# Performance work log

Hardware: AMD Instinct MI355X
Metric: run time of the kernel (lower is better)

## Reference

```python
import jax, jax.numpy as jnp
import numpy as np

FULL_SCALE = 128.0
R = 0.5
TOPK = 4


def setup_inputs() -> dict:
    key = jax.random.key(0)
    k0, k1, k2, k3, k4 = jax.random.split(key, 5)
    B, Na, Nb, D = 16, 2048, 2048, 512
    coords_a = jax.random.randint(k0, (B, Na, 3), 0, 128, dtype=jnp.int32)
    coords_b = jax.random.randint(k1, (B, Nb, 3), 0, 128, dtype=jnp.int32)
    feats_a = jax.random.normal(k2, (B, Na, D), jnp.float32)
    feats_b = jax.random.normal(k3, (B, Nb, D), jnp.float32)
    W = jax.random.normal(k4, (2 * D, D), jnp.float32) / np.sqrt(2 * D).astype(np.float32)
    bias = jnp.zeros((D,), jnp.float32)
    return {"feats_a": feats_a, "feats_b": feats_b, "W": W, "bias": bias,
            "coords_a": coords_a, "coords_b": coords_b}


def _pairwise_l2(ca, cb):
    # ca: [B,Na,3], cb: [B,Nb,3] -> [B,Na,Nb], scaled by full_scale
    x2 = jnp.sum(ca * ca, axis=-1)[:, :, None]
    y2 = jnp.sum(cb * cb, axis=-1)[:, None, :]
    sq = x2 + y2 - 2.0 * jnp.einsum('bnd,bmd->bnm', ca, cb)
    return jnp.sqrt(jnp.clip(sq, 0.0, None)) / FULL_SCALE


def reference(feats_a, feats_b, W, bias, coords_a, coords_b):
    ca = coords_a.astype(jnp.float32)
    cb = coords_b.astype(jnp.float32)
    dist = _pairwise_l2(ca, cb)                       # [B,Na,Nb]
    neg_top, idx = jax.lax.top_k(-dist, TOPK)         # smallest TOPK distances
    dist_w = R - jnp.clip(-neg_top, 0.0, R)           # [B,Na,k]
    # gather neighbor features: [B,Na,k,D]
    b_f = jnp.take_along_axis(feats_b[:, None, :, :], idx[:, :, :, None], axis=2)
    a_f = feats_a[:, :, None, :]                      # broadcast over k
    h = jnp.concatenate([b_f, a_f - b_f], axis=-1)    # [B,Na,k,2D]
    fused = jnp.sum(jax.nn.relu(h @ W + bias) * dist_w[..., None], axis=2)  # [B,Na,D]
    # ME.cat(a, tmp): concatenate features along channel dim
    return jnp.concatenate([feats_a, fused], axis=-1)  # [B,Na,2D]
```

## Files before the change

kernel.cpp:

```cpp
#include <hip/hip_runtime.h>
#include <hip/hip_bf16.h>
#include <cstdint>
#include <cstddef>

#define NA   2048
#define NB   2048
#define DD   512

typedef __attribute__((ext_vector_type(8))) short bf16x8;
typedef __attribute__((ext_vector_type(4))) float f32x4;
typedef unsigned short u16;
typedef unsigned int   u32;

__device__ __forceinline__ u16 f2b_hw(float f) {
    u32 w;
    asm("v_cvt_pk_bf16_f32 %0, %1, %2" : "=v"(w) : "v"(f), "v"(f));
    return (u16)w;
}
__device__ __forceinline__ float b2f(u16 h) {
    return __uint_as_float(((u32)h) << 16);
}
__device__ __forceinline__ u32 umin32(u32 a, u32 b) { return a < b ? a : b; }
__device__ __forceinline__ u32 umax32(u32 a, u32 b) { return a > b ? a : b; }
__device__ __forceinline__ u32 med3u(u32 a, u32 b, u32 c) {
    return umax32(umin32(a, b), umin32(umax32(a, b), c));
}
__device__ __forceinline__ bf16x8 cvt8(f32x4 v0, f32x4 v1) {
    u32 w0, w1, w2, w3;
    asm("v_cvt_pk_bf16_f32 %0, %1, %2" : "=v"(w0) : "v"(v0[0]), "v"(v0[1]));
    asm("v_cvt_pk_bf16_f32 %0, %1, %2" : "=v"(w1) : "v"(v0[2]), "v"(v0[3]));
    asm("v_cvt_pk_bf16_f32 %0, %1, %2" : "=v"(w2) : "v"(v1[0]), "v"(v1[1]));
    asm("v_cvt_pk_bf16_f32 %0, %1, %2" : "=v"(w3) : "v"(v1[2]), "v"(v1[3]));
    union { u32 u[4]; bf16x8 v; } cv;
    cv.u[0] = w0; cv.u[1] = w1; cv.u[2] = w2; cv.u[3] = w3;
    return cv.v;
}

#define GLDS16(gsrc, ldst)                                                  \
    __builtin_amdgcn_global_load_lds(                                       \
        (const __attribute__((address_space(1))) void*)(gsrc),              \
        (__attribute__((address_space(3))) void*)(ldst), 16, 0, 0)

__global__ __launch_bounds__(512) void topk_prep(
    const int* __restrict__ ca, const int* __restrict__ cb,
    int* __restrict__ idx_out, float* __restrict__ w_out,
    const float* __restrict__ fa, float* __restrict__ out,
    const float* __restrict__ W, u16* __restrict__ W2T,
    u16* __restrict__ WdT) {

    __shared__ __align__(16) char smem[33280];
    const int bid = blockIdx.x;
    const int tid = threadIdx.x;

    if (bid >= 256) {
        float (*s2)[65] = (float(*)[65])smem;
        float (*sd)[65] = (float(*)[65])(smem + 16640);
        const int pid = bid - 256;
        const int kb = (pid >> 3) * 64, nb = (pid & 7) * 64;
        const int c = tid & 63, r0 = tid >> 6;
        #pragma unroll
        for (int p = 0; p < 8; ++p) {
            int r = p * 8 + r0;
            float w1 = W[(size_t)(kb + r) * DD + nb + c];
            float w2 = W[(size_t)(512 + kb + r) * DD + nb + c];
            s2[r][c] = w2;
            sd[r][c] = w1 - w2;
        }
        __syncthreads();
        #pragma unroll
        for (int p = 0; p < 8; ++p) {
            int n = p * 8 + r0;
            W2T[(size_t)(nb + n) * DD + kb + c] = f2b_hw(s2[c][n]);
            WdT[(size_t)(nb + n) * DD + kb + c] = f2b_hw(sd[c][n]);
        }
        return;
    }

    u32* pcb  = (u32*)smem;
    u32* part = (u32*)(smem + 8192);
    const int b  = bid >> 4;
    const int i0 = (bid & 15) << 7;
    for (int p = tid; p < NB; p += 512) {
        const int* c = cb + ((size_t)b * NB + p) * 3;
        pcb[p] = (u32)c[0] | ((u32)c[1] << 8) | ((u32)c[2] << 16);
    }
    __syncthreads();

    int q = tid & 127, g = tid >> 7;
    int i = i0 + q;
    const int* ac = ca + ((size_t)b * NA + i) * 3;
    int ax = ac[0], ay = ac[1], az = ac[2];

    const float* src = fa + (size_t)bid * 128 * DD;
    float*       dst = out + (size_t)bid * 128 * 1024;

    u32 k0 = ~0u, k1 = ~0u, k2 = ~0u, k3 = ~0u;
    int j0 = g * 512;

    #pragma unroll 1
    for (int c = 0; c < 4; ++c) {
        f32x4 tr[8];
        #pragma unroll
        for (int k = 0; k < 8; ++k) {
            int f = c * 4096 + k * 512 + tid;
            tr[k] = *(const f32x4*)(src + (size_t)(f >> 7) * DD + (f & 127) * 4);
        }
        int jbase = j0 + c * 128;
        #pragma unroll 8
        for (int jj = 0; jj < 128; ++jj) {
            int j = jbase + jj;
            u32 p = pcb[j];
            int dx = ax - (int)(p & 255u);
            int dy = ay - (int)((p >> 8) & 255u);
            int dz = az - (int)(p >> 16);
            u32 s = (u32)(__mul24(dx, dx) + __mul24(dy, dy) + __mul24(dz, dz));
            u32 key = (s << 11) | (u32)j;
            u32 nk0 = umin32(k0, key);
            u32 nk1 = med3u(key, k0, k1);
            u32 nk2 = med3u(key, k1, k2);
            u32 nk3 = med3u(key, k2, k3);
            k0 = nk0; k1 = nk1; k2 = nk2; k3 = nk3;
        }
        #pragma unroll
        for (int k = 0; k < 8; ++k) {
            int f = c * 4096 + k * 512 + tid;
            *(f32x4*)(dst + (size_t)(f >> 7) * 1024 + (f & 127) * 4) = tr[k];
        }
    }

    if (g) {
        u32* pp = &part[((g - 1) * 128 + q) * 4];
        pp[0] = k0; pp[1] = k1; pp[2] = k2; pp[3] = k3;
    }
    __syncthreads();
    if (g == 0) {
        #pragma unroll
        for (int L = 0; L < 3; ++L) {
            const u32* pp = &part[(L * 128 + q) * 4];
            #pragma unroll
            for (int t = 0; t < 4; ++t) {
                u32 key = pp[t];
                u32 nk0 = umin32(k0, key);
                u32 nk1 = med3u(key, k0, k1);
                u32 nk2 = med3u(key, k1, k2);
                u32 nk3 = med3u(key, k2, k3);
                k0 = nk0; k1 = nk1; k2 = nk2; k3 = nk3;
            }
        }
        size_t o = ((size_t)b * NA + i) * 4;
        u32 ks[4] = {k0, k1, k2, k3};
        #pragma unroll
        for (int t = 0; t < 4; ++t) {
            idx_out[o + t] = (int)(ks[t] & 2047u);
            float d = sqrtf((float)(ks[t] >> 11)) * (1.0f / 128.0f);
            w_out[o + t] = 0.5f - fminf(d, 0.5f);
        }
    }
}

template<bool FUSED>
__global__ __launch_bounds__(256, 1) void gemm_kernel(
    const float* __restrict__ A, const u16* __restrict__ BT,
    u16* __restrict__ C, const int* __restrict__ idxb,
    const float* __restrict__ wb, const float* __restrict__ bias,
    const u16* __restrict__ Qb, float* __restrict__ out) {

    __shared__ __align__(16) char smem[49152];

    const int tid  = threadIdx.x;
    const int lane = tid & 63;
    const int wave = tid >> 6;
    const int mb   = blockIdx.x;
    const int m0   = FUSED ? ((((mb & 7) << 6) | (mb >> 3)) << 6) : (mb << 6);
    const int n0   = blockIdx.y << 8;
    const int l15  = lane & 15;
    const int fq   = lane >> 4;
    const int wr   = (wave >> 1) << 5;
    const int wc   = (wave & 1) << 7;

    int aflat[2]; const float* asp[2];
    #pragma unroll
    for (int i = 0; i < 2; ++i) {
        int flat = i * 256 + tid;
        int row = flat >> 3, pq = flat & 7;
        aflat[i] = flat;
        asp[i] = A + (size_t)(m0 + row) * DD + ((pq ^ (row & 7)) << 2);
    }
    int bflat[4]; const u16* bsp[4];
    #pragma unroll
    for (int i = 0; i < 4; ++i) {
        int flat = i * 256 + tid;
        int row = flat >> 2, pq = flat & 3;
        bflat[i] = flat;
        bsp[i] = BT + (size_t)(n0 + row) * DD + ((pq ^ ((row >> 1) & 3)) << 3);
    }

    int aoff[2][2], boff[8];
    #pragma unroll
    for (int mf = 0; mf < 2; ++mf) {
        int R = wr + mf * 16 + l15;
        aoff[mf][0] = R * 128 + (((2 * fq) ^ (R & 7)) << 4);
        aoff[mf][1] = R * 128 + (((2 * fq + 1) ^ (R & 7)) << 4);
    }
    #pragma unroll
    for (int nf = 0; nf < 8; ++nf) {
        int R = wc + nf * 16 + l15;
        boff[nf] = 8192 + R * 64 + ((fq ^ ((R >> 1) & 3)) << 4);
    }

    const int g16 = tid >> 4, l16 = tid & 15;
    const int r0g = g16 * 4;
    int4 iv[4];
    if (FUSED) {
        #pragma unroll
        for (int k = 0; k < 4; ++k)
            iv[k] = *(const int4*)(idxb + (size_t)(m0 + r0g + k) * 4);
    }

    f32x4 acc[2][8];
    #pragma unroll
    for (int mf = 0; mf < 2; ++mf)
        #pragma unroll
        for (int nf = 0; nf < 8; ++nf)
            acc[mf][nf] = (f32x4){0.f, 0.f, 0.f, 0.f};

#define STAGE(kk, bufb)                                                      \
    { _Pragma("unroll") for (int i = 0; i < 2; ++i)                          \
          GLDS16(asp[i] + (kk), smem + (bufb) + aflat[i] * 16);              \
      _Pragma("unroll") for (int i = 0; i < 4; ++i)                          \
          GLDS16(bsp[i] + (kk), smem + (bufb) + 8192 + bflat[i] * 16); }

    STAGE(0, 0);

    #pragma unroll 1
    for (int t = 0; t < 16; ++t) {
        const int cur = (t & 1) * 24576;
        if (t < 15) {
            STAGE((t + 1) * 32, 24576 - cur);
            asm volatile("s_waitcnt vmcnt(6)" ::: "memory");
        } else {
            asm volatile("s_waitcnt vmcnt(0)" ::: "memory");
        }
        __builtin_amdgcn_s_barrier();

        bf16x8 af[2], bfr[8];
        #pragma unroll
        for (int mf = 0; mf < 2; ++mf) {
            f32x4 lo = *(const f32x4*)(smem + cur + aoff[mf][0]);
            f32x4 hi = *(const f32x4*)(smem + cur + aoff[mf][1]);
            af[mf] = cvt8(lo, hi);
        }
        #pragma unroll
        for (int nf = 0; nf < 8; ++nf)
            bfr[nf] = *(const bf16x8*)(smem + cur + boff[nf]);
        #pragma unroll
        for (int mf = 0; mf < 2; ++mf)
            #pragma unroll
            for (int nf = 0; nf < 8; ++nf)
                acc[mf][nf] = __builtin_amdgcn_mfma_f32_16x16x32_bf16(
                    af[mf], bfr[nf], acc[mf][nf], 0, 0, 0);

        __builtin_amdgcn_s_barrier();
    }

    const int r4 = (lane >> 4) * 4;

    if (!FUSED) {
        #pragma unroll
        for (int mf = 0; mf < 2; ++mf)
            #pragma unroll
            for (int nf = 0; nf < 8; ++nf)
                #pragma unroll
                for (int j = 0; j < 4; ++j) {
                    int row = m0 + wr + mf * 16 + r4 + j;
                    int col = n0 + wc + nf * 16 + l15;
                    C[(size_t)row * DD + col] = f2b_hw(acc[mf][nf][j]);
                }
        return;
    }

    const u16* qs = Qb + ((size_t)(m0 >> 11) << 20);

    bf16x8 qA0[8], qA1[8];

#define QLOAD(BANK, k)                                                       \
    { const size_t rx = (size_t)iv[k].x * DD, ry = (size_t)iv[k].y * DD,     \
                   rz = (size_t)iv[k].z * DD, rw = (size_t)iv[k].w * DD;     \
      _Pragma("unroll") for (int cc = 0; cc < 2; ++cc) {                     \
          const int col = n0 + cc * 128 + l16 * 8;                           \
          BANK[cc*4+0] = *(const bf16x8*)(qs + rx + col);                    \
          BANK[cc*4+1] = *(const bf16x8*)(qs + ry + col);                    \
          BANK[cc*4+2] = *(const bf16x8*)(qs + rz + col);                    \
          BANK[cc*4+3] = *(const bf16x8*)(qs + rw + col);                    \
      } }

    QLOAD(qA0, 0);
    QLOAD(qA1, 1);

    float bi[8];
    #pragma unroll
    for (int nf = 0; nf < 8; ++nf)
        bi[nf] = bias[n0 + wc + nf * 16 + l15];

    u16* Ps = (u16*)smem;
    #pragma unroll
    for (int mf = 0; mf < 2; ++mf)
        #pragma unroll
        for (int nf = 0; nf < 8; ++nf)
            #pragma unroll
            for (int j = 0; j < 4; ++j)
                Ps[(wr + mf * 16 + r4 + j) * 260 + wc + nf * 16 + l15] =
                    f2b_hw(acc[mf][nf][j] + bi[nf]);
    __syncthreads();

#define QCONSUME(BANK, k)                                                    \
    { f32x4 wv = *(const f32x4*)(wb + (size_t)(m0 + r0g + (k)) * 4);         \
      _Pragma("unroll") for (int cc = 0; cc < 2; ++cc) {                     \
          const int col = cc * 128 + l16 * 8;                                \
          bf16x8 p8 = *(const bf16x8*)(Ps + (r0g + (k)) * 260 + col);        \
          float o[8];                                                        \
          _Pragma("unroll") for (int j = 0; j < 8; ++j) {                    \
              float p = b2f((u16)p8[j]);                                     \
              float s;                                                       \
              s  = fmaxf(p + b2f((u16)BANK[cc*4+0][j]), 0.f) * wv[0];        \
              s += fmaxf(p + b2f((u16)BANK[cc*4+1][j]), 0.f) * wv[1];        \
              s += fmaxf(p + b2f((u16)BANK[cc*4+2][j]), 0.f) * wv[2];        \
              s += fmaxf(p + b2f((u16)BANK[cc*4+3][j]), 0.f) * wv[3];        \
              o[j] = s;                                                      \
          }                                                                  \
          float* op = out + (size_t)(m0 + r0g + (k)) * 1024 + 512 + n0 + col;\
          *(f32x4*)op       = (f32x4){o[0], o[1], o[2], o[3]};               \
          *(f32x4*)(op + 4) = (f32x4){o[4], o[5], o[6], o[7]};               \
      } }

    QCONSUME(qA0, 0); QLOAD(qA0, 2);
    QCONSUME(qA1, 1); QLOAD(qA1, 3);
    QCONSUME(qA0, 2);
    QCONSUME(qA1, 3);
}

extern "C" void kernel_launch(void* const* d_in, const int* in_sizes, int n_in,
                              void* d_out, int out_size, void* d_ws, size_t ws_size,
                              hipStream_t stream) {
    const float* fa   = (const float*)d_in[0];
    const float* fb   = (const float*)d_in[1];
    const float* W    = (const float*)d_in[2];
    const float* bias = (const float*)d_in[3];
    const int*   ca   = (const int*)d_in[4];
    const int*   cb   = (const int*)d_in[5];
    float* out = (float*)d_out;

    char* ws = (char*)d_ws;
    u16*   Qb   = (u16*)(ws);
    u16*   W2T  = (u16*)(ws + 33554432);
    u16*   WdT  = (u16*)(ws + 34078720);
    int*   idxb = (int*)(ws + 34603008);
    float* wb   = (float*)(ws + 35127296);

    topk_prep<<<320, 512, 0, stream>>>(ca, cb, idxb, wb, fa, out,
                                       W, W2T, WdT);

    dim3 gg(512, 2);
    gemm_kernel<false><<<gg, 256, 0, stream>>>(fb, WdT, Qb, nullptr, nullptr,
                                               nullptr, nullptr, nullptr);
    gemm_kernel<true><<<gg, 256, 0, stream>>>(fa, W2T, nullptr, idxb, wb,
                                              bias, Qb, out);
}
```

Before: 124.3 us.

## Merge Q GEMM, top-k search and feature copy into one heterogeneous launch

Splits the weight transpose into its own small kernel. The Q = feats_b·Wd GEMM, the top-k neighbour search and the feats_a copy into the output then run as separate block roles inside one 1536-block launch. The aim is to overlap the ALU-bound top-k with the MFMA-bound GEMM and the bandwidth-bound copy, and to drop one kernel launch and its dependency bubble. The top-k now uses 256-thread blocks, with two thread groups each scanning 1024 candidates instead of four groups of 512. This lowers per-block parallelism for top-k, and the copy is decoupled from the top-k loop.

```diff
diff --git a/kernel.cpp b/kernel.cpp
--- a/kernel.cpp
+++ b/kernel.cpp
@@ -41,74 +41,167 @@
         (const __attribute__((address_space(1))) void*)(gsrc),              \
         (__attribute__((address_space(3))) void*)(ldst), 16, 0, 0)
 
-__global__ __launch_bounds__(512) void topk_prep(
+__global__ __launch_bounds__(512) void prep_w(const float* __restrict__ W,
+                                              u16* __restrict__ W2T,
+                                              u16* __restrict__ WdT) {
+    __shared__ __align__(16) char smem[33280];
+    float (*s2)[65] = (float(*)[65])smem;
+    float (*sd)[65] = (float(*)[65])(smem + 16640);
+    const int pid = blockIdx.x;
+    const int kb = (pid >> 3) * 64, nb = (pid & 7) * 64;
+    const int tid = threadIdx.x;
+    const int c = tid & 63, r0 = tid >> 6;
+    #pragma unroll
+    for (int p = 0; p < 8; ++p) {
+        int r = p * 8 + r0;
+        float w1 = W[(size_t)(kb + r) * DD + nb + c];
+        float w2 = W[(size_t)(512 + kb + r) * DD + nb + c];
+        s2[r][c] = w2;
+        sd[r][c] = w1 - w2;
+    }
+    __syncthreads();
+    #pragma unroll
+    for (int p = 0; p < 8; ++p) {
+        int n = p * 8 + r0;
+        W2T[(size_t)(nb + n) * DD + kb + c] = f2b_hw(s2[c][n]);
+        WdT[(size_t)(nb + n) * DD + kb + c] = f2b_hw(sd[c][n]);
+    }
+}
+
+__global__ __launch_bounds__(256, 1) void gq_tk_cp(
+    const float* __restrict__ fb, const u16* __restrict__ WdT,
+    u16* __restrict__ Qb,
     const int* __restrict__ ca, const int* __restrict__ cb,
     int* __restrict__ idx_out, float* __restrict__ w_out,
-    const float* __restrict__ fa, float* __restrict__ out,
-    const float* __restrict__ W, u16* __restrict__ W2T,
-    u16* __restrict__ WdT) {
-
-    __shared__ __align__(16) char smem[33280];
+    const float* __restrict__ fa, float* __restrict__ out) {
+
+    __shared__ __align__(16) char smem[49152];
     const int bid = blockIdx.x;
     const int tid = threadIdx.x;
 
-    if (bid >= 256) {
-        float (*s2)[65] = (float(*)[65])smem;
-        float (*sd)[65] = (float(*)[65])(smem + 16640);
-        const int pid = bid - 256;
-        const int kb = (pid >> 3) * 64, nb = (pid & 7) * 64;
-        const int c = tid & 63, r0 = tid >> 6;
-        #pragma unroll
-        for (int p = 0; p < 8; ++p) {
-            int r = p * 8 + r0;
-            float w1 = W[(size_t)(kb + r) * DD + nb + c];
-            float w2 = W[(size_t)(512 + kb + r) * DD + nb + c];
-            s2[r][c] = w2;
-            sd[r][c] = w1 - w2;
+    if (bid < 1024) {
+        const int lane = tid & 63;
+        const int wave = tid >> 6;
+        const int m0   = (bid >> 1) << 6;
+        const int n0   = (bid & 1) << 8;
+        const int l15  = lane & 15;
+        const int fq   = lane >> 4;
+        const int wr   = (wave >> 1) << 5;
+        const int wc   = (wave & 1) << 7;
+
+        int aflat[2]; const float* asp[2];
+        #pragma unroll
+        for (int i = 0; i < 2; ++i) {
+            int flat = i * 256 + tid;
+            int row = flat >> 3, pq = flat & 7;
+            aflat[i] = flat;
+            asp[i] = fb + (size_t)(m0 + row) * DD + ((pq ^ (row & 7)) << 2);
+        }
+        int bflat[4]; const u16* bsp[4];
+        #pragma unroll
+        for (int i = 0; i < 4; ++i) {
+            int flat = i * 256 + tid;
+            int row = flat >> 2, pq = flat & 3;
+            bflat[i] = flat;
+            bsp[i] = WdT + (size_t)(n0 + row) * DD
+                     + ((pq ^ ((row >> 1) & 3)) << 3);
+        }
+
+        int aoff[2][2], boff[8];
+        #pragma unroll
+        for (int mf = 0; mf < 2; ++mf) {
+            int R = wr + mf * 16 + l15;
+            aoff[mf][0] = R * 128 + (((2 * fq) ^ (R & 7)) << 4);
+            aoff[mf][1] = R * 128 + (((2 * fq + 1) ^ (R & 7)) << 4);
+        }
+        #pragma unroll
+        for (int nf = 0; nf < 8; ++nf) {
+            int R = wc + nf * 16 + l15;
+            boff[nf] = 8192 + R * 64 + ((fq ^ ((R >> 1) & 3)) << 4);
+        }
+
+        f32x4 acc[2][8];
+        #pragma unroll
+        for (int mf = 0; mf < 2; ++mf)
+            #pragma unroll
+            for (int nf = 0; nf < 8; ++nf)
+                acc[mf][nf] = (f32x4){0.f, 0.f, 0.f, 0.f};
+
+#define QSTAGE(kk, bufb)                                                     \
+    { _Pragma("unroll") for (int i = 0; i < 2; ++i)                          \
+          GLDS16(asp[i] + (kk), smem + (bufb) + aflat[i] * 16);              \
+      _Pragma("unroll") for (int i = 0; i < 4; ++i)                          \
+          GLDS16(bsp[i] + (kk), smem + (bufb) + 8192 + bflat[i] * 16); }
+
+        QSTAGE(0, 0);
+
+        #pragma unroll 1
+        for (int t = 0; t < 16; ++t) {
+            const int cur = (t & 1) * 24576;
+            if (t < 15) {
+                QSTAGE((t + 1) * 32, 24576 - cur);
+                asm volatile("s_waitcnt vmcnt(6)" ::: "memory");
+            } else {
+                asm volatile("s_waitcnt vmcnt(0)" ::: "memory");
+            }
+            __builtin_amdgcn_s_barrier();
+
+            bf16x8 af[2], bfr[8];
+            #pragma unroll
+            for (int mf = 0; mf < 2; ++mf) {
+                f32x4 lo = *(const f32x4*)(smem + cur + aoff[mf][0]);
+                f32x4 hi = *(const f32x4*)(smem + cur + aoff[mf][1]);
+                af[mf] = cvt8(lo, hi);
+            }
+            #pragma unroll
+            for (int nf = 0; nf < 8; ++nf)
+                bfr[nf] = *(const bf16x8*)(smem + cur + boff[nf]);
+            #pragma unroll
+            for (int mf = 0; mf < 2; ++mf)
+                #pragma unroll
+                for (int nf = 0; nf < 8; ++nf)
+                    acc[mf][nf] = __builtin_amdgcn_mfma_f32_16x16x32_bf16(
+                        af[mf], bfr[nf], acc[mf][nf], 0, 0, 0);
+
+            __builtin_amdgcn_s_barrier();
+        }
+
+        const int r4 = (lane >> 4) * 4;
+        #pragma unroll
+        for (int mf = 0; mf < 2; ++mf)
+            #pragma unroll
+            for (int nf = 0; nf < 8; ++nf)
+                #pragma unroll
+                for (int j = 0; j < 4; ++j) {
+                    int row = m0 + wr + mf * 16 + r4 + j;
+                    int col = n0 + wc + nf * 16 + l15;
+                    Qb[(size_t)row * DD + col] = f2b_hw(acc[mf][nf][j]);
+                }
+        return;
+    }
+
+    if (bid < 1280) {
+        u32* pcb  = (u32*)smem;
+        u32* part = (u32*)(smem + 8192);
+        const int tki = bid - 1024;
+        const int b = tki >> 4;
+        const int i0 = (tki & 15) << 7;
+        for (int p = tid; p < NB; p += 256) {
+            const int* c = cb + ((size_t)b * NB + p) * 3;
+            pcb[p] = (u32)c[0] | ((u32)c[1] << 8) | ((u32)c[2] << 16);
         }
         __syncthreads();
-        #pragma unroll
-        for (int p = 0; p < 8; ++p) {
-            int n = p * 8 + r0;
-            W2T[(size_t)(nb + n) * DD + kb + c] = f2b_hw(s2[c][n]);
-            WdT[(size_t)(nb + n) * DD + kb + c] = f2b_hw(sd[c][n]);
-        }
-        return;
-    }
-
-    u32* pcb  = (u32*)smem;
-    u32* part = (u32*)(smem + 8192);
-    const int b  = bid >> 4;
-    const int i0 = (bid & 15) << 7;
-    for (int p = tid; p < NB; p += 512) {
-        const int* c = cb + ((size_t)b * NB + p) * 3;
-        pcb[p] = (u32)c[0] | ((u32)c[1] << 8) | ((u32)c[2] << 16);
-    }
-    __syncthreads();
-
-    int q = tid & 127, g = tid >> 7;
-    int i = i0 + q;
-    const int* ac = ca + ((size_t)b * NA + i) * 3;
-    int ax = ac[0], ay = ac[1], az = ac[2];
-
-    const float* src = fa + (size_t)bid * 128 * DD;
-    float*       dst = out + (size_t)bid * 128 * 1024;
-
-    u32 k0 = ~0u, k1 = ~0u, k2 = ~0u, k3 = ~0u;
-    int j0 = g * 512;
-
-    #pragma unroll 1
-    for (int c = 0; c < 4; ++c) {
-        f32x4 tr[8];
-        #pragma unroll
-        for (int k = 0; k < 8; ++k) {
-            int f = c * 4096 + k * 512 + tid;
-            tr[k] = *(const f32x4*)(src + (size_t)(f >> 7) * DD + (f & 127) * 4);
-        }
-        int jbase = j0 + c * 128;
+
+        const int q = tid & 127, g = tid >> 7;
+        const int i = i0 + q;
+        const int* ac = ca + ((size_t)b * NA + i) * 3;
+        int ax = ac[0], ay = ac[1], az = ac[2];
+
+        u32 k0 = ~0u, k1 = ~0u, k2 = ~0u, k3 = ~0u;
+        int j0 = g << 10;
         #pragma unroll 8
-        for (int jj = 0; jj < 128; ++jj) {
-            int j = jbase + jj;
+        for (int jj = 0; jj < 1024; ++jj) {
+            int j = j0 + jj;
             u32 p = pcb[j];
             int dx = ax - (int)(p & 255u);
             int dy = ay - (int)((p >> 8) & 255u);
@@ -121,22 +214,13 @@
             u32 nk3 = med3u(key, k2, k3);
             k0 = nk0; k1 = nk1; k2 = nk2; k3 = nk3;
         }
-        #pragma unroll
-        for (int k = 0; k < 8; ++k) {
-            int f = c * 4096 + k * 512 + tid;
-            *(f32x4*)(dst + (size_t)(f >> 7) * 1024 + (f & 127) * 4) = tr[k];
-        }
-    }
-
-    if (g) {
-        u32* pp = &part[((g - 1) * 128 + q) * 4];
-        pp[0] = k0; pp[1] = k1; pp[2] = k2; pp[3] = k3;
-    }
-    __syncthreads();
-    if (g == 0) {
-        #pragma unroll
-        for (int L = 0; L < 3; ++L) {
-            const u32* pp = &part[(L * 128 + q) * 4];
+        if (g) {
+            u32* pp = &part[q * 4];
+            pp[0] = k0; pp[1] = k1; pp[2] = k2; pp[3] = k3;
+        }
+        __syncthreads();
+        if (g == 0) {
+            const u32* pp = &part[q * 4];
             #pragma unroll
             for (int t = 0; t < 4; ++t) {
                 u32 key = pp[t];
@@ -146,14 +230,32 @@
                 u32 nk3 = med3u(key, k2, k3);
                 k0 = nk0; k1 = nk1; k2 = nk2; k3 = nk3;
             }
-        }
-        size_t o = ((size_t)b * NA + i) * 4;
-        u32 ks[4] = {k0, k1, k2, k3};
-        #pragma unroll
-        for (int t = 0; t < 4; ++t) {
-            idx_out[o + t] = (int)(ks[t] & 2047u);
-            float d = sqrtf((float)(ks[t] >> 11)) * (1.0f / 128.0f);
-            w_out[o + t] = 0.5f - fminf(d, 0.5f);
+            size_t o = ((size_t)b * NA + i) * 4;
+            u32 ks[4] = {k0, k1, k2, k3};
+            #pragma unroll
+            for (int t = 0; t < 4; ++t) {
+                idx_out[o + t] = (int)(ks[t] & 2047u);
+                float d = sqrtf((float)(ks[t] >> 11)) * (1.0f / 128.0f);
+                w_out[o + t] = 0.5f - fminf(d, 0.5f);
+            }
+        }
+        return;
+    }
+
+    {
+        const int cid = bid - 1280;
+        const float* src = fa + ((size_t)cid << 16);
+        float*       dst = out + ((size_t)cid << 17);
+        #pragma unroll 4
+        for (int it = 0; it < 32; ++it) {
+            int flat = it * 256 + tid;
+            int row = flat >> 6, c8 = (flat & 63) << 3;
+            const float* s = src + ((size_t)row << 9) + c8;
+            f32x4 v0 = *(const f32x4*)s;
+            f32x4 v1 = *(const f32x4*)(s + 4);
+            float* d = dst + ((size_t)row << 10) + c8;
+            *(f32x4*)d = v0;
+            *(f32x4*)(d + 4) = v1;
         }
     }
 }
@@ -357,12 +459,11 @@
     int*   idxb = (int*)(ws + 34603008);
     float* wb   = (float*)(ws + 35127296);
 
-    topk_prep<<<320, 512, 0, stream>>>(ca, cb, idxb, wb, fa, out,
-                                       W, W2T, WdT);
+    prep_w<<<64, 512, 0, stream>>>(W, W2T, WdT);
+
+    gq_tk_cp<<<1536, 256, 0, stream>>>(fb, WdT, Qb, ca, cb, idxb, wb, fa, out);
 
     dim3 gg(512, 2);
-    gemm_kernel<false><<<gg, 256, 0, stream>>>(fb, WdT, Qb, nullptr, nullptr,
-                                               nullptr, nullptr, nullptr);
     gemm_kernel<true><<<gg, 256, 0, stream>>>(fa, W2T, nullptr, idxb, wb,
                                               bias, Qb, out);
 }
```

After: 136.7 us. 1.1x slower.
